# Kernel optimization log

Hardware: AMD Instinct MI355X
Metric: run time of the kernel (lower is better)

Reference implementation:

```python
import jax, jax.numpy as jnp
import numpy as np

D_MODEL = 1024
N_HEADS = 16
D_HEAD = D_MODEL // N_HEADS
B, T = 4, 2048


def setup_inputs() -> dict:
    key = jax.random.key(0)
    k1, k2, k3 = jax.random.split(key, 3)
    x = jax.random.normal(k1, (B, T, D_MODEL), dtype=jnp.float32)
    # match nn.Linear init scale roughly (uniform ~ 1/sqrt(fan_in)); scale normal for stability
    w_qkv = jax.random.normal(k2, (D_MODEL, 3 * D_MODEL), dtype=jnp.float32) / np.sqrt(D_MODEL)
    w_out = jax.random.normal(k3, (D_MODEL, D_MODEL), dtype=jnp.float32) / np.sqrt(D_MODEL)
    return {"x": x, "w_qkv": w_qkv, "w_out": w_out}


def reference(x, w_qkv, w_out):
    Bx, Tx, D = x.shape
    H, Dh = N_HEADS, D_HEAD
    qkv = x @ w_qkv                                  # [B,T,3D]
    qkv = qkv.reshape(Bx, Tx, 3, H, Dh)
    q, k, v = qkv[:, :, 0], qkv[:, :, 1], qkv[:, :, 2]  # [B,T,H,Dh]
    scores = jnp.einsum('bqhd,bkhd->bhqk', q, k) / np.sqrt(Dh).astype(np.float32)
    mask = jnp.triu(jnp.ones((Tx, Tx), dtype=bool), k=1)  # causal: mask future
    scores = jnp.where(mask, -jnp.inf, scores)
    attn = jax.nn.softmax(scores, axis=-1)
    out = jnp.einsum('bhqk,bkhd->bqhd', attn, v).reshape(Bx, Tx, D)
    return out @ w_out
```

## Files before the change

### kernel.cpp

```cpp
#include <hip/hip_runtime.h>
#include <math.h>

#define T_SEQ 2048
#define NB 4
#define NH 16
#define DH 64
#define DM 1024

typedef __attribute__((ext_vector_type(8))) __bf16 bf16x8;
typedef __attribute__((ext_vector_type(4))) float f32x4;

typedef const __attribute__((address_space(1))) void* gas_t;
typedef __attribute__((address_space(3))) void* las_t;

__device__ inline bool detect_f32(const unsigned short* probe, int lane) {
    unsigned short u = probe[lane];
    int e = (u >> 7) & 0xFF;
    bool outlier = (e >= 140) || (e <= 90 && (u & 0x7fff) != 0);
    unsigned long long m = __ballot(outlier);
    return __popcll(m) >= 4;
}

__device__ inline bf16x8 load8_flex(const void* base, long elem, bool f32) {
    if (!f32) {
        return *(const bf16x8*)((const __bf16*)base + elem);
    } else {
        const float* f = (const float*)base + elem;
        float4 a = *(const float4*)f;
        float4 b = *(const float4*)(f + 4);
        bf16x8 r;
        r[0] = (__bf16)a.x; r[1] = (__bf16)a.y; r[2] = (__bf16)a.z; r[3] = (__bf16)a.w;
        r[4] = (__bf16)b.x; r[5] = (__bf16)b.y; r[6] = (__bf16)b.z; r[7] = (__bf16)b.w;
        return r;
    }
}

__global__ __launch_bounds__(256)
void cvt_x(const float* __restrict__ in, __bf16* __restrict__ out, long n8) {
    long i = (long)blockIdx.x * blockDim.x + threadIdx.x;
    if (i >= n8) return;
    const float* f = in + i * 8;
    float4 a = *(const float4*)f;
    float4 b = *(const float4*)(f + 4);
    bf16x8 r;
    r[0] = (__bf16)a.x; r[1] = (__bf16)a.y; r[2] = (__bf16)a.z; r[3] = (__bf16)a.w;
    r[4] = (__bf16)b.x; r[5] = (__bf16)b.y; r[6] = (__bf16)b.z; r[7] = (__bf16)b.w;
    *(bf16x8*)(out + i * 8) = r;
}

__global__ __launch_bounds__(256)
void tpose_cvt(const float* __restrict__ in, __bf16* __restrict__ out, int R, int C) {
    __shared__ __bf16 tile[32][33];
    const int bx = blockIdx.x * 32;
    const int by = blockIdx.y * 32;
    const int tx = threadIdx.x & 31;
    const int ty = threadIdx.x >> 5;
#pragma unroll
    for (int it = 0; it < 4; ++it) {
        int r = ty + it * 8;
        tile[r][tx] = (__bf16)in[(long)(by + r) * C + bx + tx];
    }
    __syncthreads();
#pragma unroll
    for (int it = 0; it < 4; ++it) {
        int r = ty + it * 8;
        out[(long)(bx + r) * R + by + tx] = tile[tx][r];
    }
}

__global__ __launch_bounds__(256)
void gemm_bt(const __bf16* __restrict__ A, long lda,
             const __bf16* __restrict__ Bt, long ldb,
             void* __restrict__ C, long ldc, int c_f32, int K) {
    __shared__ __align__(16) __bf16 sA[128 * 32];
    __shared__ __align__(16) __bf16 sB[128 * 32];
    const int tid  = threadIdx.x;
    const int lane = tid & 63;
    const int wave = tid >> 6;
    const int l15  = lane & 15;
    const int quad = lane >> 4;
    const int bm = blockIdx.y * 128;
    const int bn = blockIdx.x * 128;
    const int wm = (wave & 1) * 64;
    const int wn = (wave >> 1) * 64;

    f32x4 zero = {0.f, 0.f, 0.f, 0.f};
    f32x4 acc[4][4];
#pragma unroll
    for (int i = 0; i < 4; ++i)
#pragma unroll
        for (int j = 0; j < 4; ++j) acc[i][j] = zero;

    const int srow = tid >> 2;
    const int scol = (tid & 3) * 8;
    const __bf16* gA0 = A  + (long)(bm + srow) * lda + scol;
    const __bf16* gA1 = A  + (long)(bm + 64 + srow) * lda + scol;
    const __bf16* gB0 = Bt + (long)(bn + srow) * ldb + scol;
    const __bf16* gB1 = Bt + (long)(bn + 64 + srow) * ldb + scol;

    __bf16* lA0 = sA + wave * 512;
    __bf16* lA1 = sA + 2048 + wave * 512;
    __bf16* lB0 = sB + wave * 512;
    __bf16* lB1 = sB + 2048 + wave * 512;

    for (int k0 = 0; k0 < K; k0 += 32) {
        __syncthreads();
        __builtin_amdgcn_global_load_lds((gas_t)(gA0 + k0), (las_t)lA0, 16, 0, 0);
        __builtin_amdgcn_global_load_lds((gas_t)(gA1 + k0), (las_t)lA1, 16, 0, 0);
        __builtin_amdgcn_global_load_lds((gas_t)(gB0 + k0), (las_t)lB0, 16, 0, 0);
        __builtin_amdgcn_global_load_lds((gas_t)(gB1 + k0), (las_t)lB1, 16, 0, 0);
        __syncthreads();

        bf16x8 af[4], bfm[4];
#pragma unroll
        for (int i = 0; i < 4; ++i)
            af[i] = *(const bf16x8*)(sA + (wm + i * 16 + l15) * 32 + quad * 8);
#pragma unroll
        for (int j = 0; j < 4; ++j)
            bfm[j] = *(const bf16x8*)(sB + (wn + j * 16 + l15) * 32 + quad * 8);
#pragma unroll
        for (int i = 0; i < 4; ++i)
#pragma unroll
            for (int j = 0; j < 4; ++j)
                acc[i][j] = __builtin_amdgcn_mfma_f32_16x16x32_bf16(af[i], bfm[j], acc[i][j], 0, 0, 0);
    }

#pragma unroll
    for (int i = 0; i < 4; ++i)
#pragma unroll
        for (int j = 0; j < 4; ++j)
#pragma unroll
            for (int r = 0; r < 4; ++r) {
                int row = bm + wm + i * 16 + quad * 4 + r;
                int col = bn + wn + j * 16 + l15;
                if (c_f32)
                    ((float*)C)[(long)row * ldc + col] = acc[i][j][r];
                else
                    ((__bf16*)C)[(long)row * ldc + col] = (__bf16)acc[i][j][r];
            }
}

__global__ __launch_bounds__(256)
void gemm_bn(const void* __restrict__ A, long lda, long a0, int a_flex,
             const void* __restrict__ B, long ldb, int b_flex,
             void* __restrict__ C, long ldc, int c_flex, int K,
             const unsigned short* __restrict__ probe) {
    __shared__ __align__(16) __bf16 sA[128 * 32];
    __shared__ __align__(16) __bf16 sB[128 * 32];
    const int tid  = threadIdx.x;
    const int lane = tid & 63;
    const int wave = tid >> 6;
    const int l15  = lane & 15;
    const int quad = lane >> 4;
    const int bm = blockIdx.y * 128;
    const int bn = blockIdx.x * 128;
    const int wm = (wave & 1) * 64;
    const int wn = (wave >> 1) * 64;

    const bool is_f32 = detect_f32(probe, lane);
    const bool a_f32 = a_flex && is_f32;
    const bool b_f32 = b_flex && is_f32;
    const bool c_f32 = c_flex && is_f32;

    f32x4 zero = {0.f, 0.f, 0.f, 0.f};
    f32x4 acc[4][4];
#pragma unroll
    for (int i = 0; i < 4; ++i)
#pragma unroll
        for (int j = 0; j < 4; ++j) acc[i][j] = zero;

    const int srow = tid >> 2;
    const int scol = (tid & 3) * 8;

    for (int k0 = 0; k0 < K; k0 += 32) {
        __syncthreads();
        *(bf16x8*)(sA + tid * 8) =
            load8_flex(A, a0 + (long)(bm + srow) * lda + k0 + scol, a_f32);
        *(bf16x8*)(sA + 2048 + tid * 8) =
            load8_flex(A, a0 + (long)(bm + 64 + srow) * lda + k0 + scol, a_f32);
#pragma unroll
        for (int it = 0; it < 2; ++it) {
            int idx = tid + it * 256;
            int kk  = idx & 31;
            int n8  = (idx >> 5) * 8;
            bf16x8 bv = load8_flex(B, (long)(k0 + kk) * ldb + bn + n8, b_f32);
#pragma unroll
            for (int jj = 0; jj < 8; ++jj) sB[(n8 + jj) * 32 + kk] = bv[jj];
        }
        __syncthreads();

        bf16x8 af[4], bfm[4];
#pragma unroll
        for (int i = 0; i < 4; ++i)
            af[i] = *(const bf16x8*)(sA + (wm + i * 16 + l15) * 32 + quad * 8);
#pragma unroll
        for (int j = 0; j < 4; ++j)
            bfm[j] = *(const bf16x8*)(sB + (wn + j * 16 + l15) * 32 + quad * 8);
#pragma unroll
        for (int i = 0; i < 4; ++i)
#pragma unroll
            for (int j = 0; j < 4; ++j)
                acc[i][j] = __builtin_amdgcn_mfma_f32_16x16x32_bf16(af[i], bfm[j], acc[i][j], 0, 0, 0);
    }

#pragma unroll
    for (int i = 0; i < 4; ++i)
#pragma unroll
        for (int j = 0; j < 4; ++j)
#pragma unroll
            for (int r = 0; r < 4; ++r) {
                int row = bm + wm + i * 16 + quad * 4 + r;
                int col = bn + wn + j * 16 + l15;
                if (c_f32)
                    ((float*)C)[(long)row * ldc + col] = acc[i][j][r];
                else
                    ((__bf16*)C)[(long)row * ldc + col] = (__bf16)acc[i][j][r];
            }
}

__global__ __launch_bounds__(512, 4)
void attn_k(__bf16* __restrict__ qkvp, int bhbits) {
    const int bid  = blockIdx.x;
    const int p    = bid >> bhbits;
    const int bh   = bid & ((1 << bhbits) - 1);
    const int h    = bh & 15;
    const int b    = bh >> 4;
    const int tid  = threadIdx.x;
    const int lane = tid & 63;
    const int wave = tid >> 6;
    const int l15  = lane & 15;
    const int quad = lane >> 4;

    __shared__ __align__(16) __bf16 sK[64 * 72];
    __shared__ __align__(16) __bf16 sVT[64 * 64];
    __shared__ __align__(16) __bf16 sP[8][16 * 64];

    const long rs = 3 * DM;
    __bf16* base = qkvp + (long)b * T_SEQ * rs + h * DH;

    const int sr  = tid >> 3;
    const int sm  = tid & 7;
    const int sc8 = sm * 8;
    const int rot = 8 * ((5 * sm) & 7);
    const int vcol = (sr + rot) & 63;

    bf16x8 vone;
#pragma unroll
    for (int jj = 0; jj < 8; ++jj) vone[jj] = (__bf16)1.0f;

    f32x4 zero = {0.f, 0.f, 0.f, 0.f};

#pragma unroll 1
    for (int half = 0; half < 2; ++half) {
        const int qt  = half ? (15 - p) : p;
        const int q0  = qt * 128;
        const int wq0 = q0 + wave * 16;
        const int nk  = (q0 + 128) >> 6;

        bf16x8 qa[2];
#pragma unroll
        for (int kk = 0; kk < 2; ++kk) {
            bf16x8 v = *(const bf16x8*)(base + (long)(wq0 + l15) * rs + kk * 32 + quad * 8);
#pragma unroll
            for (int jj = 0; jj < 8; ++jj) v[jj] = (__bf16)((float)v[jj] * 0.125f);
            qa[kk] = v;
        }

        f32x4 o[4], o4;
        o4 = zero;
#pragma unroll
        for (int j = 0; j < 4; ++j) o[j] = zero;

        bf16x8 kreg, vreg;
        {
            const __bf16* rp = base + (long)sr * rs;
            kreg = *(const bf16x8*)(rp + DM + sc8);
            vreg = *(const bf16x8*)(rp + 2 * DM + sc8);
        }

        for (int t = 0; t < nk; ++t) {
            const int k0 = t * 64;
            __syncthreads();
            *(bf16x8*)(sK + sr * 72 + sc8) = kreg;
#pragma unroll
            for (int jj = 0; jj < 8; ++jj)
                sVT[(sc8 + jj) * 64 + vcol] = vreg[jj];
            __syncthreads();

            if (t + 1 < nk) {
                const __bf16* rp = base + (long)(k0 + 64 + sr) * rs;
                kreg = *(const bf16x8*)(rp + DM + sc8);
                vreg = *(const bf16x8*)(rp + 2 * DM + sc8);
            }

            const bool active = (k0 <= wq0 + 15);
            if (active) {
                f32x4 s[4];
#pragma unroll
                for (int j = 0; j < 4; ++j) s[j] = zero;
#pragma unroll
                for (int kk = 0; kk < 2; ++kk) {
                    bf16x8 kb[4];
#pragma unroll
                    for (int j = 0; j < 4; ++j)
                        kb[j] = *(const bf16x8*)(sK + (j * 16 + l15) * 72 + kk * 32 + quad * 8);
#pragma unroll
                    for (int j = 0; j < 4; ++j)
                        s[j] = __builtin_amdgcn_mfma_f32_16x16x32_bf16(qa[kk], kb[j], s[j], 0, 0, 0);
                }

                const bool needmask = (k0 + 63 > wq0);
#pragma unroll
                for (int r = 0; r < 4; ++r) {
                    const int qg = wq0 + quad * 4 + r;
#pragma unroll
                    for (int j = 0; j < 4; ++j) {
                        const int kg = k0 + j * 16 + l15;
                        float pv = __expf(fminf(s[j][r], 60.f));
                        if (needmask) pv = (kg > qg) ? 0.f : pv;
                        sP[wave][(quad * 4 + r) * 64 +
                                 ((j * 16 + l15 + 16 * quad) & 63)] = (__bf16)pv;
                    }
                }
            }

            __builtin_amdgcn_sched_barrier(0);
            __builtin_amdgcn_s_waitcnt(0xc07f);
            __builtin_amdgcn_sched_barrier(0);

            if (active) {
#pragma unroll
                for (int kk = 0; kk < 2; ++kk) {
                    bf16x8 pa, vb[4];
                    pa = *(const bf16x8*)(
                        &sP[wave][l15 * 64 +
                                  ((kk * 32 + quad * 8 + 16 * (l15 >> 2)) & 63)]);
#pragma unroll
                    for (int j = 0; j < 4; ++j) {
                        const int g = (2 * j + (l15 >> 3)) & 7;
                        vb[j] = *(const bf16x8*)(
                            sVT + (j * 16 + l15) * 64 +
                            ((kk * 32 + quad * 8 + 8 * ((5 * g) & 7)) & 63));
                    }
#pragma unroll
                    for (int j = 0; j < 4; ++j)
                        o[j] = __builtin_amdgcn_mfma_f32_16x16x32_bf16(pa, vb[j], o[j], 0, 0, 0);
                    o4 = __builtin_amdgcn_mfma_f32_16x16x32_bf16(pa, vone, o4, 0, 0, 0);
                }
            }
        }

#pragma unroll
        for (int r = 0; r < 4; ++r) {
            const int qg  = wq0 + quad * 4 + r;
            const float inv = 1.f / o4[r];
#pragma unroll
            for (int j = 0; j < 4; ++j)
                base[(long)qg * rs + j * 16 + l15] = (__bf16)(o[j][r] * inv);
        }
    }
}

__global__ __launch_bounds__(256)
void fallback_k(float* __restrict__ out, long n, float wsmb) {
    long i = (long)blockIdx.x * blockDim.x + threadIdx.x;
    for (; i < n; i += (long)gridDim.x * blockDim.x) out[i] = 0.f;
    if (blockIdx.x == 0 && threadIdx.x == 0) out[0] = wsmb;
}

extern "C" void kernel_launch(void* const* d_in, const int* in_sizes, int n_in,
                              void* d_out, int out_size, void* d_ws, size_t ws_size,
                              hipStream_t stream) {
    const void* x     = d_in[0];
    const void* w_qkv = d_in[1];
    const void* w_out = d_in[2];
    const unsigned short* probe = (const unsigned short*)d_in[0];

    __bf16* qkv = (__bf16*)d_ws;
    __bf16* xb  = qkv + (size_t)8192 * 3072;
    __bf16* wtq = xb  + (size_t)8192 * 1024;
    __bf16* wto = wtq + (size_t)3072 * 1024;

    const size_t NEED_T1   = (size_t)72 * 1024 * 1024;
    const size_t NEED_FULL = (size_t)8192 * 3072 * 2;
    const size_t NEED_B    = (size_t)2048 * 3072 * 2;

    if (ws_size >= NEED_T1) {
        cvt_x<<<dim3(4096), 256, 0, stream>>>((const float*)x, xb, (long)8192 * 1024 / 8);
        tpose_cvt<<<dim3(96, 32), 256, 0, stream>>>((const float*)w_qkv, wtq, 1024, 3072);
        tpose_cvt<<<dim3(32, 32), 256, 0, stream>>>((const float*)w_out, wto, 1024, 1024);
        gemm_bt<<<dim3(24, 64), 256, 0, stream>>>(xb, 1024, wtq, 1024, qkv, 3072, 0, 1024);
        attn_k<<<dim3(8 * 64), 512, 0, stream>>>(qkv, 6);
        gemm_bt<<<dim3(8, 64), 256, 0, stream>>>(qkv, 3072, wto, 1024, d_out, 1024, 1, 1024);
    } else if (ws_size >= NEED_FULL) {
        gemm_bn<<<dim3(24, 64), 256, 0, stream>>>(
            x, 1024, 0, 1, w_qkv, 3072, 1, qkv, 3072, 0, 1024, probe);
        attn_k<<<dim3(8 * 64), 512, 0, stream>>>(qkv, 6);
        gemm_bn<<<dim3(8, 64), 256, 0, stream>>>(
            qkv, 3072, 0, 0, w_out, 1024, 1, d_out, 1024, 1, 1024, probe);
    } else if (ws_size >= NEED_B) {
        for (int b = 0; b < NB; ++b) {
            long xoff = (long)b * T_SEQ * DM;
            gemm_bn<<<dim3(24, 16), 256, 0, stream>>>(
                x, 1024, xoff, 1, w_qkv, 3072, 1, qkv, 3072, 0, 1024, probe);
            attn_k<<<dim3(8 * 16), 512, 0, stream>>>(qkv, 4);
            gemm_bn<<<dim3(8, 16), 256, 0, stream>>>(
                qkv, 3072, 0, 0, w_out, 1024, 1,
                (void*)((char*)d_out + (size_t)b * T_SEQ * DM * 4),
                1024, 1, 1024, probe);
        }
    } else {
        fallback_k<<<dim3(512), 256, 0, stream>>>(
            (float*)d_out, (long)8192 * 1024, (float)(ws_size >> 20));
    }
}
```

Baseline: 282.6 us.

## Process both causal query tiles in a single K/V pass and use exp2

The attention kernel used to walk the K/V sequence twice, once for the low query tile and once for the paired high tile. It now keeps both tiles' Q fragments and accumulators live and streams K/V only once, up to the high tile's extent. Each staged K/V block in shared memory then serves both tiles, which halves K/V global loads and the barriers spent re-staging them. The softmax switches to exp2 with log2(e) folded into the Q scale. The costs are higher register pressure from doubled accumulators, with a risk of spills or lower occupancy under launch_bounds(512,4), and a larger sP buffer.

```diff
diff --git a/kernel.cpp b/kernel.cpp
--- a/kernel.cpp
+++ b/kernel.cpp
@@ -12,6 +12,12 @@
 
 typedef const __attribute__((address_space(1))) void* gas_t;
 typedef __attribute__((address_space(3))) void* las_t;
+
+#if __has_builtin(__builtin_amdgcn_exp2f)
+#define EXP2(x) __builtin_amdgcn_exp2f(x)
+#else
+#define EXP2(x) __expf((x) * 0.69314718056f)
+#endif
 
 __device__ inline bool detect_f32(const unsigned short* probe, int lane) {
     unsigned short u = probe[lane];
@@ -233,7 +239,7 @@
 
     __shared__ __align__(16) __bf16 sK[64 * 72];
     __shared__ __align__(16) __bf16 sVT[64 * 64];
-    __shared__ __align__(16) __bf16 sP[8][16 * 64];
+    __shared__ __align__(16) __bf16 sP[8][32 * 64];
 
     const long rs = 3 * DM;
     __bf16* base = qkvp + (long)b * T_SEQ * rs + h * DH;
@@ -250,113 +256,161 @@
 
     f32x4 zero = {0.f, 0.f, 0.f, 0.f};
 
-#pragma unroll 1
-    for (int half = 0; half < 2; ++half) {
-        const int qt  = half ? (15 - p) : p;
-        const int q0  = qt * 128;
-        const int wq0 = q0 + wave * 16;
-        const int nk  = (q0 + 128) >> 6;
-
-        bf16x8 qa[2];
-#pragma unroll
-        for (int kk = 0; kk < 2; ++kk) {
-            bf16x8 v = *(const bf16x8*)(base + (long)(wq0 + l15) * rs + kk * 32 + quad * 8);
-#pragma unroll
-            for (int jj = 0; jj < 8; ++jj) v[jj] = (__bf16)((float)v[jj] * 0.125f);
-            qa[kk] = v;
-        }
-
-        f32x4 o[4], o4;
-        o4 = zero;
-#pragma unroll
-        for (int j = 0; j < 4; ++j) o[j] = zero;
-
-        bf16x8 kreg, vreg;
-        {
-            const __bf16* rp = base + (long)sr * rs;
+    const int qt_lo = p;
+    const int qt_hi = 15 - p;
+    const int wq_lo = qt_lo * 128 + wave * 16;
+    const int wq_hi = qt_hi * 128 + wave * 16;
+    const int nk_hi = 2 * qt_hi + 2;
+
+    const float qscale = 0.125f * 1.44269504089f;
+    bf16x8 qa_lo[2], qa_hi[2];
+#pragma unroll
+    for (int kk = 0; kk < 2; ++kk) {
+        bf16x8 v = *(const bf16x8*)(base + (long)(wq_lo + l15) * rs + kk * 32 + quad * 8);
+        bf16x8 w = *(const bf16x8*)(base + (long)(wq_hi + l15) * rs + kk * 32 + quad * 8);
+#pragma unroll
+        for (int jj = 0; jj < 8; ++jj) {
+            v[jj] = (__bf16)((float)v[jj] * qscale);
+            w[jj] = (__bf16)((float)w[jj] * qscale);
+        }
+        qa_lo[kk] = v;
+        qa_hi[kk] = w;
+    }
+
+    f32x4 o_lo[4], o_hi[4], o4_lo, o4_hi;
+    o4_lo = zero; o4_hi = zero;
+#pragma unroll
+    for (int j = 0; j < 4; ++j) { o_lo[j] = zero; o_hi[j] = zero; }
+
+    bf16x8 kreg, vreg;
+    {
+        const __bf16* rp = base + (long)sr * rs;
+        kreg = *(const bf16x8*)(rp + DM + sc8);
+        vreg = *(const bf16x8*)(rp + 2 * DM + sc8);
+    }
+
+    for (int t = 0; t < nk_hi; ++t) {
+        const int k0 = t * 64;
+        __syncthreads();
+        *(bf16x8*)(sK + sr * 72 + sc8) = kreg;
+#pragma unroll
+        for (int jj = 0; jj < 8; ++jj)
+            sVT[(sc8 + jj) * 64 + vcol] = vreg[jj];
+        __syncthreads();
+
+        if (t + 1 < nk_hi) {
+            const __bf16* rp = base + (long)(k0 + 64 + sr) * rs;
             kreg = *(const bf16x8*)(rp + DM + sc8);
             vreg = *(const bf16x8*)(rp + 2 * DM + sc8);
         }
 
-        for (int t = 0; t < nk; ++t) {
-            const int k0 = t * 64;
-            __syncthreads();
-            *(bf16x8*)(sK + sr * 72 + sc8) = kreg;
-#pragma unroll
-            for (int jj = 0; jj < 8; ++jj)
-                sVT[(sc8 + jj) * 64 + vcol] = vreg[jj];
-            __syncthreads();
-
-            if (t + 1 < nk) {
-                const __bf16* rp = base + (long)(k0 + 64 + sr) * rs;
-                kreg = *(const bf16x8*)(rp + DM + sc8);
-                vreg = *(const bf16x8*)(rp + 2 * DM + sc8);
-            }
-
-            const bool active = (k0 <= wq0 + 15);
-            if (active) {
-                f32x4 s[4];
-#pragma unroll
-                for (int j = 0; j < 4; ++j) s[j] = zero;
-#pragma unroll
-                for (int kk = 0; kk < 2; ++kk) {
-                    bf16x8 kb[4];
-#pragma unroll
-                    for (int j = 0; j < 4; ++j)
-                        kb[j] = *(const bf16x8*)(sK + (j * 16 + l15) * 72 + kk * 32 + quad * 8);
-#pragma unroll
-                    for (int j = 0; j < 4; ++j)
-                        s[j] = __builtin_amdgcn_mfma_f32_16x16x32_bf16(qa[kk], kb[j], s[j], 0, 0, 0);
+        const bool act_lo = (k0 <= wq_lo + 15);
+        const bool act_hi = (k0 <= wq_hi + 15);
+
+        if (act_lo) {
+            f32x4 s[4];
+#pragma unroll
+            for (int j = 0; j < 4; ++j) s[j] = zero;
+#pragma unroll
+            for (int kk = 0; kk < 2; ++kk) {
+                bf16x8 kb[4];
+#pragma unroll
+                for (int j = 0; j < 4; ++j)
+                    kb[j] = *(const bf16x8*)(sK + (j * 16 + l15) * 72 + kk * 32 + quad * 8);
+#pragma unroll
+                for (int j = 0; j < 4; ++j)
+                    s[j] = __builtin_amdgcn_mfma_f32_16x16x32_bf16(qa_lo[kk], kb[j], s[j], 0, 0, 0);
+            }
+            const bool needmask = (k0 + 63 > wq_lo);
+#pragma unroll
+            for (int r = 0; r < 4; ++r) {
+                const int qg = wq_lo + quad * 4 + r;
+#pragma unroll
+                for (int j = 0; j < 4; ++j) {
+                    const int kg = k0 + j * 16 + l15;
+                    float pv = EXP2(fminf(s[j][r], 86.f));
+                    if (needmask) pv = (kg > qg) ? 0.f : pv;
+                    sP[wave][(quad * 4 + r) * 64 +
+                             ((j * 16 + l15 + 16 * quad) & 63)] = (__bf16)pv;
                 }
-
-                const bool needmask = (k0 + 63 > wq0);
-#pragma unroll
-                for (int r = 0; r < 4; ++r) {
-                    const int qg = wq0 + quad * 4 + r;
-#pragma unroll
-                    for (int j = 0; j < 4; ++j) {
-                        const int kg = k0 + j * 16 + l15;
-                        float pv = __expf(fminf(s[j][r], 60.f));
-                        if (needmask) pv = (kg > qg) ? 0.f : pv;
-                        sP[wave][(quad * 4 + r) * 64 +
-                                 ((j * 16 + l15 + 16 * quad) & 63)] = (__bf16)pv;
-                    }
+            }
+        }
+        if (act_hi) {
+            f32x4 s[4];
+#pragma unroll
+            for (int j = 0; j < 4; ++j) s[j] = zero;
+#pragma unroll
+            for (int kk = 0; kk < 2; ++kk) {
+                bf16x8 kb[4];
+#pragma unroll
+                for (int j = 0; j < 4; ++j)
+                    kb[j] = *(const bf16x8*)(sK + (j * 16 + l15) * 72 + kk * 32 + quad * 8);
+#pragma unroll
+                for (int j = 0; j < 4; ++j)
+                    s[j] = __builtin_amdgcn_mfma_f32_16x16x32_bf16(qa_hi[kk], kb[j], s[j], 0, 0, 0);
+            }
+            const bool needmask = (k0 + 63 > wq_hi);
+#pragma unroll
+            for (int r = 0; r < 4; ++r) {
+                const int qg = wq_hi + quad * 4 + r;
+#pragma unroll
+                for (int j = 0; j < 4; ++j) {
+                    const int kg = k0 + j * 16 + l15;
+                    float pv = EXP2(fminf(s[j][r], 86.f));
+                    if (needmask) pv = (kg > qg) ? 0.f : pv;
+                    sP[wave][(16 + quad * 4 + r) * 64 +
+                             ((j * 16 + l15 + 16 * quad) & 63)] = (__bf16)pv;
                 }
             }
-
-            __builtin_amdgcn_sched_barrier(0);
-            __builtin_amdgcn_s_waitcnt(0xc07f);
-            __builtin_amdgcn_sched_barrier(0);
-
-            if (active) {
-#pragma unroll
-                for (int kk = 0; kk < 2; ++kk) {
-                    bf16x8 pa, vb[4];
-                    pa = *(const bf16x8*)(
+        }
+
+        __builtin_amdgcn_sched_barrier(0);
+        __builtin_amdgcn_s_waitcnt(0xc07f);
+        __builtin_amdgcn_sched_barrier(0);
+
+        if (act_lo || act_hi) {
+#pragma unroll
+            for (int kk = 0; kk < 2; ++kk) {
+                bf16x8 vb[4];
+#pragma unroll
+                for (int j = 0; j < 4; ++j) {
+                    const int g = (2 * j + (l15 >> 3)) & 7;
+                    vb[j] = *(const bf16x8*)(
+                        sVT + (j * 16 + l15) * 64 +
+                        ((kk * 32 + quad * 8 + 8 * ((5 * g) & 7)) & 63));
+                }
+                if (act_lo) {
+                    bf16x8 pa = *(const bf16x8*)(
                         &sP[wave][l15 * 64 +
                                   ((kk * 32 + quad * 8 + 16 * (l15 >> 2)) & 63)]);
 #pragma unroll
-                    for (int j = 0; j < 4; ++j) {
-                        const int g = (2 * j + (l15 >> 3)) & 7;
-                        vb[j] = *(const bf16x8*)(
-                            sVT + (j * 16 + l15) * 64 +
-                            ((kk * 32 + quad * 8 + 8 * ((5 * g) & 7)) & 63));
-                    }
-#pragma unroll
                     for (int j = 0; j < 4; ++j)
-                        o[j] = __builtin_amdgcn_mfma_f32_16x16x32_bf16(pa, vb[j], o[j], 0, 0, 0);
-                    o4 = __builtin_amdgcn_mfma_f32_16x16x32_bf16(pa, vone, o4, 0, 0, 0);
+                        o_lo[j] = __builtin_amdgcn_mfma_f32_16x16x32_bf16(pa, vb[j], o_lo[j], 0, 0, 0);
+                    o4_lo = __builtin_amdgcn_mfma_f32_16x16x32_bf16(pa, vone, o4_lo, 0, 0, 0);
                 }
-            }
-        }
-
-#pragma unroll
-        for (int r = 0; r < 4; ++r) {
-            const int qg  = wq0 + quad * 4 + r;
-            const float inv = 1.f / o4[r];
-#pragma unroll
-            for (int j = 0; j < 4; ++j)
-                base[(long)qg * rs + j * 16 + l15] = (__bf16)(o[j][r] * inv);
+                if (act_hi) {
+                    bf16x8 pa = *(const bf16x8*)(
+                        &sP[wave][(16 + l15) * 64 +
+                                  ((kk * 32 + quad * 8 + 16 * (l15 >> 2)) & 63)]);
+#pragma unroll
+                    for (int j = 0; j < 4; ++j)
+                        o_hi[j] = __builtin_amdgcn_mfma_f32_16x16x32_bf16(pa, vb[j], o_hi[j], 0, 0, 0);
+                    o4_hi = __builtin_amdgcn_mfma_f32_16x16x32_bf16(pa, vone, o4_hi, 0, 0, 0);
+                }
+            }
+        }
+    }
+
+#pragma unroll
+    for (int r = 0; r < 4; ++r) {
+        const int qg_lo = wq_lo + quad * 4 + r;
+        const int qg_hi = wq_hi + quad * 4 + r;
+        const float inv_lo = 1.f / o4_lo[r];
+        const float inv_hi = 1.f / o4_hi[r];
+#pragma unroll
+        for (int j = 0; j < 4; ++j) {
+            base[(long)qg_lo * rs + j * 16 + l15] = (__bf16)(o_lo[j][r] * inv_lo);
+            base[(long)qg_hi * rs + j * 16 + l15] = (__bf16)(o_hi[j][r] * inv_hi);
         }
     }
 }
```

Measured after the change: 286.3 us. Within noise of the previous version (+1.3%).
